# Kernel optimization log

Measured on AMD Instinct MI355X. Metric: run time of the kernel, lower is better.

Reference implementation:

```python
import jax, jax.numpy as jnp
import numpy as np

EPS = 1e-12

def lap_kernel(x, y, sigma):
    # x: [N,d], y: [M,d] -> exp(-||x-y|| / sigma), [N,M]
    D = jnp.sum((x[:, None, :] - y[None, :, :]) ** 2, axis=-1)
    return jnp.exp(-jnp.sqrt(jnp.maximum(D, EPS)) / sigma)

def setup_inputs() -> dict:
    key = jax.random.key(0)
    ks = jax.random.split(key, 8)
    N, L, NN, D, H = 20000, 7, 2048, 3, 16
    inp = {
        'x': jax.random.uniform(ks[0], (N, D), dtype=jnp.float32),
        'trial_points': jax.random.uniform(ks[1], (L, NN, D), dtype=jnp.float32),
        'W_emb': jax.random.normal(ks[2], (L, NN, H), dtype=jnp.float32),
        'alpha': 0.001 * jnp.ones((L,), dtype=jnp.float32),
        'sigma': 0.1 * jnp.ones((L,), dtype=jnp.float32),
    }
    dims = [L * H, 40, 40, 40, 40, 1]
    for i in range(5):
        fan_in = dims[i]
        kw = jax.random.fold_in(ks[3], i)
        inp[f'w{i+1}'] = (jax.random.normal(kw, (dims[i], dims[i+1]), dtype=jnp.float32)
                          / np.sqrt(fan_in).astype(np.float32))
        inp[f'b{i+1}'] = jnp.zeros((dims[i+1],), dtype=jnp.float32)
    return inp

def reference(x, trial_points, W_emb, alpha, sigma, w1, b1, w2, b2, w3, b3, w4, b4, w5, b5):
    n_lvls, n_nodes = trial_points.shape[0], trial_points.shape[1]
    I = jnp.eye(n_nodes, dtype=x.dtype)
    hs = []
    for l in range(n_lvls):  # fixed small loop over levels (7)
        xt = trial_points[l]                         # [NN, d]
        K_xx = lap_kernel(xt, xt, sigma[l])          # [NN, NN]
        a = jnp.linalg.solve(K_xx + alpha[l] * I, W_emb[l])  # ridge solve
        K_tx = lap_kernel(x, xt, sigma[l])           # [N, NN]
        hs.append(K_tx @ a)                          # [N, H]
    h = jnp.concatenate(hs, axis=-1)                 # [N, 7*H]
    z = jax.nn.relu(h @ w1 + b1)
    z = jax.nn.relu(z @ w2 + b2)
    z = jax.nn.relu(z @ w3 + b3)
    z = jax.nn.relu(z @ w4 + b4)
    return z @ w5 + b5
```

## Files before the change

kernel.cpp:

```cpp
#include <hip/hip_runtime.h>
#include <math.h>

#define NN   2048
#define NLVL 7
#define HD   16
#define HTOT 112
#define NB   64

__global__ __launch_bounds__(256) void build_K(
    const float* __restrict__ tp, const float* __restrict__ alpha,
    const float* __restrict__ sigma, float* __restrict__ K, int lvl0)
{
  int lz  = blockIdx.y;
  int lvl = lvl0 + lz;
  int idx = blockIdx.x * 256 + threadIdx.x;
  int i = idx >> 11, j = idx & (NN - 1);
  const float* xt = tp + (size_t)lvl * NN * 3;
  float xi0 = xt[i*3+0], xi1 = xt[i*3+1], xi2 = xt[i*3+2];
  float xj0 = xt[j*3+0], xj1 = xt[j*3+1], xj2 = xt[j*3+2];
  float d0 = xi0-xj0, d1 = xi1-xj1, d2 = xi2-xj2;
  float dd = d0*d0 + d1*d1 + d2*d2;
  float v = __expf(-sqrtf(fmaxf(dd, 1e-12f)) / sigma[lvl]);
  if (i == j) v += alpha[lvl];
  K[(size_t)lz*NN*NN + idx] = v;
}

__global__ __launch_bounds__(64) void chol_diag(float* __restrict__ K, int k)
{
  int lz = blockIdx.x;
  float* A = K + (size_t)lz * NN * NN;
  __shared__ float s[64][65];
  int tid = threadIdx.x;
  #pragma unroll 4
  for (int r = 0; r < 64; ++r)
    s[r][tid] = A[(size_t)(k + r) * NN + k + tid];
  __syncthreads();
  for (int j = 0; j < 64; ++j) {
    float djj = s[j][j];
    float inv = 1.0f / sqrtf(djj);
    if (tid > j) s[tid][j] *= inv;
    __syncthreads();
    if (tid > j) {
      float fr = s[tid][j];
      for (int p = j + 1; p <= tid; ++p)
        s[tid][p] -= fr * s[p][j];
    }
    __syncthreads();
  }
  s[tid][tid] = sqrtf(s[tid][tid]);
  __syncthreads();
  #pragma unroll 4
  for (int r = 0; r < 64; ++r)
    A[(size_t)(k + r) * NN + k + tid] = s[r][tid];
}

__global__ __launch_bounds__(128) void panel_trsm(float* __restrict__ K, int k)
{
  int lz = blockIdx.y;
  float* A = K + (size_t)lz * NN * NN;
  __shared__ float Ld[64][65];
  __shared__ float invd[64];
  __shared__ float P[128][65];
  int tid = threadIdx.x;
  for (int t = tid; t < 4096; t += 128)
    Ld[t >> 6][t & 63] = A[(size_t)(k + (t >> 6)) * NN + k + (t & 63)];
  int rbase = k + NB + blockIdx.x * 128;
  for (int t = tid; t < 128 * 64; t += 128) {
    int r = t >> 6, c = t & 63;
    if (rbase + r < NN) P[r][c] = A[(size_t)(rbase + r) * NN + k + c];
  }
  __syncthreads();
  if (tid < 64) invd[tid] = 1.0f / Ld[tid][tid];
  __syncthreads();
  int r = tid;
  if (rbase + r < NN) {
    for (int j = 0; j < 64; ++j) {
      float acc = P[r][j];
      for (int p = 0; p < j; ++p) acc -= Ld[j][p] * P[r][p];
      P[r][j] = acc * invd[j];
    }
  }
  __syncthreads();
  for (int t = tid; t < 128 * 64; t += 128) {
    int rr = t >> 6, c = t & 63;
    if (rbase + rr < NN) A[(size_t)(rbase + rr) * NN + k + c] = P[rr][c];
  }
}

__global__ __launch_bounds__(256) void syrk_update(float* __restrict__ K, int k)
{
  if (blockIdx.y > blockIdx.x) return;
  int lz = blockIdx.z;
  float* A = K + (size_t)lz * NN * NN;
  int i0 = k + NB + blockIdx.x * 64;
  int j0 = k + NB + blockIdx.y * 64;
  __shared__ __align__(16) float Asub[64][68];
  __shared__ __align__(16) float Bsub[64][68];
  int tid = threadIdx.x;
  for (int t = tid; t < 4096; t += 256) {
    int r = t >> 6, c = t & 63;
    Asub[r][c] = A[(size_t)(i0 + r) * NN + k + c];
    Bsub[r][c] = A[(size_t)(j0 + r) * NN + k + c];
  }
  __syncthreads();
  int tx = tid & 15, ty = tid >> 4;
  float acc[4][4] = {{0.f}};
  #pragma unroll
  for (int p4 = 0; p4 < 16; ++p4) {
    float4 av[4], bv[4];
    #pragma unroll
    for (int ii = 0; ii < 4; ++ii) av[ii] = *(const float4*)&Asub[ty*4+ii][p4*4];
    #pragma unroll
    for (int jj = 0; jj < 4; ++jj) bv[jj] = *(const float4*)&Bsub[tx*4+jj][p4*4];
    #pragma unroll
    for (int ii = 0; ii < 4; ++ii)
      #pragma unroll
      for (int jj = 0; jj < 4; ++jj)
        acc[ii][jj] += av[ii].x*bv[jj].x + av[ii].y*bv[jj].y
                     + av[ii].z*bv[jj].z + av[ii].w*bv[jj].w;
  }
  #pragma unroll
  for (int ii = 0; ii < 4; ++ii) {
    int row = i0 + ty*4 + ii;
    float4* cp = (float4*)&A[(size_t)row * NN + j0 + tx*4];
    float4 cv = *cp;
    cv.x -= acc[ii][0]; cv.y -= acc[ii][1]; cv.z -= acc[ii][2]; cv.w -= acc[ii][3];
    *cp = cv;
  }
}

__global__ __launch_bounds__(512) void trsm_diag_fwd(
    const float* __restrict__ K, float* __restrict__ Y, int kb)
{
  int lz = blockIdx.x;
  const float* L = K + (size_t)lz * NN * NN;
  float* y = Y + (size_t)lz * NN * HD;
  __shared__ float Ld1[64][65];
  __shared__ float L21[64][65];
  __shared__ float Ld2[64][65];
  __shared__ float yb[128][HD];
  int tid = threadIdx.x;
  for (int t = tid; t < 4096; t += 512) {
    int r = t >> 6, c = t & 63;
    Ld1[r][c] = L[(size_t)(kb + r) * NN + kb + c];
    L21[r][c] = L[(size_t)(kb + 64 + r) * NN + kb + c];
    Ld2[r][c] = L[(size_t)(kb + 64 + r) * NN + kb + 64 + c];
  }
  for (int t = tid; t < 128 * HD; t += 512)
    yb[t >> 4][t & 15] = y[(size_t)kb * HD + t];
  __syncthreads();
  if (tid < HD) {
    int c = tid;
    for (int j = 0; j < 64; ++j) {
      float acc = yb[j][c];
      for (int p = 0; p < j; ++p) acc -= Ld1[j][p] * yb[p][c];
      yb[j][c] = acc / Ld1[j][j];
    }
  }
  __syncthreads();
  {
    int o = tid;
    #pragma unroll
    for (int q = 0; q < 2; ++q, o += 512) {
      int r = o >> 4, c = o & 15;
      float acc = 0.f;
      #pragma unroll 16
      for (int p = 0; p < 64; ++p) acc += L21[r][p] * yb[p][c];
      yb[64 + r][c] -= acc;
    }
  }
  __syncthreads();
  if (tid < HD) {
    int c = tid;
    for (int j = 0; j < 64; ++j) {
      float acc = yb[64 + j][c];
      for (int p = 0; p < j; ++p) acc -= Ld2[j][p] * yb[64 + p][c];
      yb[64 + j][c] = acc / Ld2[j][j];
    }
  }
  __syncthreads();
  for (int t = tid; t < 128 * HD; t += 512)
    y[(size_t)kb * HD + t] = yb[t >> 4][t & 15];
}

__global__ __launch_bounds__(256) void trsm_upd_fwd(
    const float* __restrict__ K, float* __restrict__ Y, int kb)
{
  int lz = blockIdx.y;
  const float* L = K + (size_t)lz * NN * NN;
  float* y = Y + (size_t)lz * NN * HD;
  int i0 = kb + 128 + blockIdx.x * 64;
  __shared__ float Lt[64][129];
  __shared__ __align__(16) float yk[128][HD];
  int tid = threadIdx.x;
  for (int e = tid; e < 64 * 128; e += 256) {
    int r = e >> 7, p = e & 127;
    Lt[r][p] = L[(size_t)(i0 + r) * NN + kb + p];
  }
  for (int e = tid; e < 128 * HD; e += 256)
    yk[e >> 4][e & 15] = y[(size_t)kb * HD + e];
  __syncthreads();
  int row = tid & 63, cg = tid >> 6;
  float4 acc = make_float4(0.f, 0.f, 0.f, 0.f);
  #pragma unroll 8
  for (int p = 0; p < 128; ++p) {
    float l = Lt[row][p];
    float4 yv = *(const float4*)&yk[p][cg * 4];
    acc.x += l * yv.x; acc.y += l * yv.y; acc.z += l * yv.z; acc.w += l * yv.w;
  }
  float4* yp = (float4*)&y[(size_t)(i0 + row) * HD + cg * 4];
  float4 cv = *yp;
  cv.x -= acc.x; cv.y -= acc.y; cv.z -= acc.z; cv.w -= acc.w;
  *yp = cv;
}

__global__ __launch_bounds__(512) void trsm_diag_bwd(
    const float* __restrict__ K, float* __restrict__ Y, int kb)
{
  int lz = blockIdx.x;
  const float* L = K + (size_t)lz * NN * NN;
  float* y = Y + (size_t)lz * NN * HD;
  __shared__ float Ld1[64][65];
  __shared__ float L21[64][65];
  __shared__ float Ld2[64][65];
  __shared__ float yb[128][HD];
  int tid = threadIdx.x;
  for (int t = tid; t < 4096; t += 512) {
    int r = t >> 6, c = t & 63;
    Ld1[r][c] = L[(size_t)(kb + r) * NN + kb + c];
    L21[r][c] = L[(size_t)(kb + 64 + r) * NN + kb + c];
    Ld2[r][c] = L[(size_t)(kb + 64 + r) * NN + kb + 64 + c];
  }
  for (int t = tid; t < 128 * HD; t += 512)
    yb[t >> 4][t & 15] = y[(size_t)kb * HD + t];
  __syncthreads();
  if (tid < HD) {
    int c = tid;
    for (int j = 63; j >= 0; --j) {
      float acc = yb[64 + j][c];
      for (int p = j + 1; p < 64; ++p) acc -= Ld2[p][j] * yb[64 + p][c];
      yb[64 + j][c] = acc / Ld2[j][j];
    }
  }
  __syncthreads();
  {
    int o = tid;
    #pragma unroll
    for (int q = 0; q < 2; ++q, o += 512) {
      int r = o >> 4, c = o & 15;
      float acc = 0.f;
      #pragma unroll 16
      for (int p = 0; p < 64; ++p) acc += L21[p][r] * yb[64 + p][c];
      yb[r][c] -= acc;
    }
  }
  __syncthreads();
  if (tid < HD) {
    int c = tid;
    for (int j = 63; j >= 0; --j) {
      float acc = yb[j][c];
      for (int p = j + 1; p < 64; ++p) acc -= Ld1[p][j] * yb[p][c];
      yb[j][c] = acc / Ld1[j][j];
    }
  }
  __syncthreads();
  for (int t = tid; t < 128 * HD; t += 512)
    y[(size_t)kb * HD + t] = yb[t >> 4][t & 15];
}

__global__ __launch_bounds__(256) void trsm_upd_bwd(
    const float* __restrict__ K, float* __restrict__ Y, int kb)
{
  int lz = blockIdx.y;
  const float* L = K + (size_t)lz * NN * NN;
  float* y = Y + (size_t)lz * NN * HD;
  int i0 = blockIdx.x * 64;
  __shared__ float Lt[64][129];
  __shared__ __align__(16) float yk[128][HD];
  int tid = threadIdx.x;
  for (int e = tid; e < 64 * 128; e += 256) {
    int p = e >> 6, r = e & 63;
    Lt[r][p] = L[(size_t)(kb + p) * NN + i0 + r];
  }
  for (int e = tid; e < 128 * HD; e += 256)
    yk[e >> 4][e & 15] = y[(size_t)kb * HD + e];
  __syncthreads();
  int row = tid & 63, cg = tid >> 6;
  float4 acc = make_float4(0.f, 0.f, 0.f, 0.f);
  #pragma unroll 8
  for (int p = 0; p < 128; ++p) {
    float l = Lt[row][p];
    float4 yv = *(const float4*)&yk[p][cg * 4];
    acc.x += l * yv.x; acc.y += l * yv.y; acc.z += l * yv.z; acc.w += l * yv.w;
  }
  float4* yp = (float4*)&y[(size_t)(i0 + row) * HD + cg * 4];
  float4 cv = *yp;
  cv.x -= acc.x; cv.y -= acc.y; cv.z -= acc.z; cv.w -= acc.w;
  *yp = cv;
}

__global__ __launch_bounds__(256) void compute_h(
    const float* __restrict__ x, const float* __restrict__ tp,
    const float* __restrict__ A, const float* __restrict__ sigma,
    float* __restrict__ Ht, int N)
{
  int l = blockIdx.y;
  const float* xt = tp + (size_t)l * NN * 3;
  const float* al = A + (size_t)l * NN * HD;
  float inv_sigma = 1.0f / sigma[l];
  int tid = threadIdx.x;
  int r0 = blockIdx.x * 512 + tid;
  int r1 = r0 + 256;
  float x00=0.f,x01=0.f,x02=0.f, x10=0.f,x11=0.f,x12=0.f;
  if (r0 < N) { x00 = x[r0*3]; x01 = x[r0*3+1]; x02 = x[r0*3+2]; }
  if (r1 < N) { x10 = x[r1*3]; x11 = x[r1*3+1]; x12 = x[r1*3+2]; }
  __shared__ float sxt[128*3];
  __shared__ __align__(16) float sa[128*16];
  float acc0[16] = {0.f}; float acc1[16] = {0.f};
  for (int jc = 0; jc < NN; jc += 128) {
    __syncthreads();
    for (int t = tid; t < 384; t += 256)  sxt[t] = xt[jc*3 + t];
    for (int t = tid; t < 2048; t += 256) sa[t]  = al[jc*16 + t];
    __syncthreads();
    for (int jl = 0; jl < 128; ++jl) {
      float t0 = sxt[jl*3+0], t1 = sxt[jl*3+1], t2 = sxt[jl*3+2];
      float da = x00 - t0, db = x01 - t1, dc = x02 - t2;
      float d20 = da*da + db*db + dc*dc;
      da = x10 - t0; db = x11 - t1; dc = x12 - t2;
      float d21 = da*da + db*db + dc*dc;
      float k0 = __expf(-sqrtf(fmaxf(d20, 1e-12f)) * inv_sigma);
      float k1 = __expf(-sqrtf(fmaxf(d21, 1e-12f)) * inv_sigma);
      const float4* a4 = (const float4*)&sa[jl*16];
      #pragma unroll
      for (int q = 0; q < 4; ++q) {
        float4 av = a4[q];
        acc0[q*4+0] += k0*av.x; acc0[q*4+1] += k0*av.y;
        acc0[q*4+2] += k0*av.z; acc0[q*4+3] += k0*av.w;
        acc1[q*4+0] += k1*av.x; acc1[q*4+1] += k1*av.y;
        acc1[q*4+2] += k1*av.z; acc1[q*4+3] += k1*av.w;
      }
    }
  }
  if (r0 < N) {
    #pragma unroll
    for (int hh = 0; hh < 16; ++hh) Ht[(size_t)(l*HD + hh) * N + r0] = acc0[hh];
  }
  if (r1 < N) {
    #pragma unroll
    for (int hh = 0; hh < 16; ++hh) Ht[(size_t)(l*HD + hh) * N + r1] = acc1[hh];
  }
}

__global__ __launch_bounds__(256) void mlp_kernel(
    const float* __restrict__ Ht,
    const float* __restrict__ w1, const float* __restrict__ b1,
    const float* __restrict__ w2, const float* __restrict__ b2,
    const float* __restrict__ w3, const float* __restrict__ b3,
    const float* __restrict__ w4, const float* __restrict__ b4,
    const float* __restrict__ w5, const float* __restrict__ b5,
    float* __restrict__ out, int N)
{
  __shared__ __align__(16) float W1[HTOT*40];
  __shared__ __align__(16) float W2[1600];
  __shared__ __align__(16) float W3[1600];
  __shared__ __align__(16) float W4[1600];
  __shared__ float W5[40], B1[40], B2[40], B3[40], B4[40];
  __shared__ float B5s;
  int tid = threadIdx.x;
  for (int t = tid; t < HTOT*40; t += 256) W1[t] = w1[t];
  for (int t = tid; t < 1600; t += 256) { W2[t] = w2[t]; W3[t] = w3[t]; W4[t] = w4[t]; }
  if (tid < 40) { B1[tid]=b1[tid]; B2[tid]=b2[tid]; B3[tid]=b3[tid]; B4[tid]=b4[tid]; W5[tid]=w5[tid]; }
  if (tid == 0) B5s = b5[0];
  __syncthreads();
  int r = blockIdx.x * 256 + tid;
  if (r >= N) return;

  float za[40], zb[40];
  #pragma unroll
  for (int o = 0; o < 40; ++o) za[o] = B1[o];
  for (int i = 0; i < HTOT; ++i) {
    float hv = Ht[(size_t)i * N + r];
    const float4* wp = (const float4*)&W1[i*40];
    #pragma unroll
    for (int q = 0; q < 10; ++q) {
      float4 wv = wp[q];
      za[q*4+0] += hv*wv.x; za[q*4+1] += hv*wv.y; za[q*4+2] += hv*wv.z; za[q*4+3] += hv*wv.w;
    }
  }
  #pragma unroll
  for (int o = 0; o < 40; ++o) { za[o] = fmaxf(za[o], 0.f); zb[o] = B2[o]; }
  for (int i = 0; i < 40; ++i) {
    float hv = za[i];
    const float4* wp = (const float4*)&W2[i*40];
    #pragma unroll
    for (int q = 0; q < 10; ++q) {
      float4 wv = wp[q];
      zb[q*4+0] += hv*wv.x; zb[q*4+1] += hv*wv.y; zb[q*4+2] += hv*wv.z; zb[q*4+3] += hv*wv.w;
    }
  }
  #pragma unroll
  for (int o = 0; o < 40; ++o) { zb[o] = fmaxf(zb[o], 0.f); za[o] = B3[o]; }
  for (int i = 0; i < 40; ++i) {
    float hv = zb[i];
    const float4* wp = (const float4*)&W3[i*40];
    #pragma unroll
    for (int q = 0; q < 10; ++q) {
      float4 wv = wp[q];
      za[q*4+0] += hv*wv.x; za[q*4+1] += hv*wv.y; za[q*4+2] += hv*wv.z; za[q*4+3] += hv*wv.w;
    }
  }
  #pragma unroll
  for (int o = 0; o < 40; ++o) { za[o] = fmaxf(za[o], 0.f); zb[o] = B4[o]; }
  for (int i = 0; i < 40; ++i) {
    float hv = za[i];
    const float4* wp = (const float4*)&W4[i*40];
    #pragma unroll
    for (int q = 0; q < 10; ++q) {
      float4 wv = wp[q];
      zb[q*4+0] += hv*wv.x; zb[q*4+1] += hv*wv.y; zb[q*4+2] += hv*wv.z; zb[q*4+3] += hv*wv.w;
    }
  }
  float ov = B5s;
  #pragma unroll
  for (int o = 0; o < 40; ++o) ov += fmaxf(zb[o], 0.f) * W5[o];
  out[r] = ov;
}

static void run_chol_steps(float* K, int nl, hipStream_t stream)
{
  for (int k = 0; k < NN; k += NB) {
    chol_diag<<<nl, 64, 0, stream>>>(K, k);
    int m = NN - k - NB;
    if (m > 0) {
      panel_trsm<<<dim3((m + 127) / 128, nl), 128, 0, stream>>>(K, k);
      int t = m / 64;
      syrk_update<<<dim3(t, t, nl), 256, 0, stream>>>(K, k);
    }
  }
}

static void run_trsm_steps(const float* K, float* Y, int nl, hipStream_t stream)
{
  for (int kb = 0; kb < NN; kb += 128) {
    trsm_diag_fwd<<<nl, 512, 0, stream>>>(K, Y, kb);
    int m = NN - kb - 128;
    if (m > 0)
      trsm_upd_fwd<<<dim3(m / 64, nl), 256, 0, stream>>>(K, Y, kb);
  }
  for (int kb = NN - 128; kb >= 0; kb -= 128) {
    trsm_diag_bwd<<<nl, 512, 0, stream>>>(K, Y, kb);
    if (kb > 0)
      trsm_upd_bwd<<<dim3(kb / 64, nl), 256, 0, stream>>>(K, Y, kb);
  }
}

extern "C" void kernel_launch(void* const* d_in, const int* in_sizes, int n_in,
                              void* d_out, int out_size, void* d_ws, size_t ws_size,
                              hipStream_t stream)
{
  (void)n_in; (void)out_size;
  const float* x     = (const float*)d_in[0];
  const float* tp    = (const float*)d_in[1];
  const float* W     = (const float*)d_in[2];
  const float* alpha = (const float*)d_in[3];
  const float* sigma = (const float*)d_in[4];
  const float* w1 = (const float*)d_in[5];  const float* b1 = (const float*)d_in[6];
  const float* w2 = (const float*)d_in[7];  const float* b2 = (const float*)d_in[8];
  const float* w3 = (const float*)d_in[9];  const float* b3 = (const float*)d_in[10];
  const float* w4 = (const float*)d_in[11]; const float* b4 = (const float*)d_in[12];
  const float* w5 = (const float*)d_in[13]; const float* b5 = (const float*)d_in[14];
  float* out = (float*)d_out;
  int N = in_sizes[0] / 3;

  size_t kElems1 = (size_t)NN * NN;
  size_t aElems  = (size_t)NLVL * NN * HD;
  size_t hElems  = (size_t)N * HTOT;
  size_t need7   = (7 * kElems1 + aElems + hElems) * sizeof(float);
  bool batched = ws_size >= need7;
  int nlK = batched ? NLVL : 1;

  float* K = (float*)d_ws;
  float* A = K + (size_t)nlK * kElems1;
  float* H = A + aElems;

  hipMemcpyAsync(A, W, aElems * sizeof(float), hipMemcpyDeviceToDevice, stream);

  if (batched) {
    build_K<<<dim3((unsigned)(kElems1 / 256), NLVL), 256, 0, stream>>>(tp, alpha, sigma, K, 0);
    run_chol_steps(K, NLVL, stream);
    run_trsm_steps(K, A, NLVL, stream);
  } else {
    for (int l = 0; l < NLVL; ++l) {
      build_K<<<dim3((unsigned)(kElems1 / 256), 1), 256, 0, stream>>>(tp, alpha, sigma, K, l);
      run_chol_steps(K, 1, stream);
      run_trsm_steps(K, A + (size_t)l * NN * HD, 1, stream);
    }
  }

  compute_h<<<dim3((N + 511) / 512, NLVL), 256, 0, stream>>>(x, tp, A, sigma, H, N);
  mlp_kernel<<<(N + 255) / 256, 256, 0, stream>>>(H, w1, b1, w2, b2, w3, b3, w4, b4, w5, b5, out, N);
}
```

Baseline: 9.309 ms.

## Fuse kernel build, Cholesky and triangular solves into one cooperative persistent kernel

Replaces the many per-step launches for building the kernel matrices, the blocked Cholesky factorisation and the forward/backward triangular solves with a single cooperative grid kernel that uses grid-wide syncs between phases. Diagonal factorisation is fused into the trailing SYRK step, and diagonal solves are fused with their updates on dedicated blocks per level. This targets launch overhead and idle gaps on the long serial dependency chain, at the cost of grid-sync latency and limited occupancy. It also changes compute_h to one row per thread with more blocks, and falls back to the old path if the cooperative launch fails.

```diff
diff --git a/kernel.cpp b/kernel.cpp
--- a/kernel.cpp
+++ b/kernel.cpp
@@ -1,11 +1,429 @@
 #include <hip/hip_runtime.h>
+#include <hip/hip_cooperative_groups.h>
 #include <math.h>
 
-#define NN   2048
-#define NLVL 7
-#define HD   16
-#define HTOT 112
-#define NB   64
+namespace cg = cooperative_groups;
+
+#define NN     2048
+#define NLVL   7
+#define HD     16
+#define HTOT   112
+#define NB     64
+
+#define LDS_FLOATS 10368
+
+__device__ void chol64_lds(float* s, int tid)
+{
+  for (int j = 0; j < 64; ++j) {
+    float pj = s[j*68+j];
+    __syncthreads();
+    float inv = 1.0f / sqrtf(pj);
+    if (tid == j) s[j*68+j] = sqrtf(pj);
+    else if (tid > j && tid < 64) s[tid*68+j] *= inv;
+    __syncthreads();
+    int rr = j + 1 + (tid >> 2);
+    if (rr < 64) {
+      float lr = s[rr*68+j];
+      for (int c = j + 1 + (tid & 3); c <= rr; c += 4)
+        s[rr*68+c] -= lr * s[c*68+j];
+    }
+    __syncthreads();
+  }
+}
+
+__device__ void panel_tile(float* __restrict__ A, int k, int r0, float* lds, int tid)
+{
+  float* Ld = lds; float* P = lds + 4160; float* invd = lds + 8320;
+  for (int t = tid; t < 4096; t += 256) {
+    int r = t >> 6, c = t & 63;
+    Ld[r*65+c] = A[(size_t)(k + r) * NN + k + c];
+    P [r*65+c] = A[(size_t)(r0 + r) * NN + k + c];
+  }
+  __syncthreads();
+  if (tid < 64) invd[tid] = 1.0f / Ld[tid*65+tid];
+  __syncthreads();
+  if (tid < 64) {
+    int r = tid;
+    for (int j = 0; j < 64; ++j) {
+      float acc = P[r*65+j];
+      for (int p = 0; p < j; ++p) acc -= Ld[j*65+p] * P[r*65+p];
+      P[r*65+j] = acc * invd[j];
+    }
+  }
+  __syncthreads();
+  for (int t = tid; t < 4096; t += 256) {
+    int r = t >> 6, c = t & 63;
+    A[(size_t)(r0 + r) * NN + k + c] = P[r*65+c];
+  }
+  __syncthreads();
+}
+
+__device__ void syrk_tile(float* __restrict__ A, int k, int i0, int j0,
+                          float* lds, int tid, bool fuse)
+{
+  float* As = lds; float* Bs = lds + 4352;
+  for (int t = tid; t < 4096; t += 256) {
+    int r = t >> 6, c = t & 63;
+    As[r*68+c] = A[(size_t)(i0 + r) * NN + k + c];
+    Bs[r*68+c] = A[(size_t)(j0 + r) * NN + k + c];
+  }
+  __syncthreads();
+  int tx = tid & 15, ty = tid >> 4;
+  float acc[4][4] = {{0.f}};
+  #pragma unroll
+  for (int p4 = 0; p4 < 16; ++p4) {
+    float4 av[4], bv[4];
+    #pragma unroll
+    for (int ii = 0; ii < 4; ++ii) av[ii] = *(const float4*)&As[(ty*4+ii)*68 + p4*4];
+    #pragma unroll
+    for (int jj = 0; jj < 4; ++jj) bv[jj] = *(const float4*)&Bs[(tx*4+jj)*68 + p4*4];
+    #pragma unroll
+    for (int ii = 0; ii < 4; ++ii)
+      #pragma unroll
+      for (int jj = 0; jj < 4; ++jj)
+        acc[ii][jj] += av[ii].x*bv[jj].x + av[ii].y*bv[jj].y
+                     + av[ii].z*bv[jj].z + av[ii].w*bv[jj].w;
+  }
+  if (!fuse) {
+    #pragma unroll
+    for (int ii = 0; ii < 4; ++ii) {
+      float4* cp = (float4*)&A[(size_t)(i0 + ty*4 + ii) * NN + j0 + tx*4];
+      float4 cv = *cp;
+      cv.x -= acc[ii][0]; cv.y -= acc[ii][1]; cv.z -= acc[ii][2]; cv.w -= acc[ii][3];
+      *cp = cv;
+    }
+    __syncthreads();
+  } else {
+    float4 cv[4];
+    #pragma unroll
+    for (int ii = 0; ii < 4; ++ii) {
+      cv[ii] = *(const float4*)&A[(size_t)(i0 + ty*4 + ii) * NN + j0 + tx*4];
+      cv[ii].x -= acc[ii][0]; cv[ii].y -= acc[ii][1];
+      cv[ii].z -= acc[ii][2]; cv[ii].w -= acc[ii][3];
+    }
+    __syncthreads();
+    #pragma unroll
+    for (int ii = 0; ii < 4; ++ii)
+      *(float4*)&As[(ty*4+ii)*68 + tx*4] = cv[ii];
+    __syncthreads();
+    chol64_lds(As, tid);
+    for (int t = tid; t < 4096; t += 256) {
+      int r = t >> 6, c = t & 63;
+      A[(size_t)(i0 + r) * NN + i0 + c] = As[r*68+c];
+    }
+    __syncthreads();
+  }
+}
+
+__device__ void solve128_fwd(const float* __restrict__ L, int kb, float* lds, int tid)
+{
+  float* LA = lds; float* LB = lds + 4160; float* yb = lds + 8320;
+  for (int t = tid; t < 4096; t += 256) {
+    int r = t >> 6, c = t & 63;
+    LA[r*65+c] = L[(size_t)(kb + r) * NN + kb + c];
+    LB[r*65+c] = L[(size_t)(kb + 64 + r) * NN + kb + c];
+  }
+  __syncthreads();
+  if (tid < HD) {
+    int c = tid;
+    for (int j = 0; j < 64; ++j) {
+      float acc = yb[j*HD + c];
+      for (int p = 0; p < j; ++p) acc -= LA[j*65+p] * yb[p*HD + c];
+      yb[j*HD + c] = acc / LA[j*65+j];
+    }
+  }
+  __syncthreads();
+  for (int o = tid; o < 1024; o += 256) {
+    int r = o >> 4, c = o & 15;
+    float acc = 0.f;
+    #pragma unroll 8
+    for (int p = 0; p < 64; ++p) acc += LB[r*65+p] * yb[p*HD + c];
+    yb[(64+r)*HD + c] -= acc;
+  }
+  for (int t = tid; t < 4096; t += 256) {
+    int r = t >> 6, c = t & 63;
+    LA[r*65+c] = L[(size_t)(kb + 64 + r) * NN + (kb + 64) + c];
+  }
+  __syncthreads();
+  if (tid < HD) {
+    int c = tid;
+    for (int j = 0; j < 64; ++j) {
+      float acc = yb[(64+j)*HD + c];
+      for (int p = 0; p < j; ++p) acc -= LA[j*65+p] * yb[(64+p)*HD + c];
+      yb[(64+j)*HD + c] = acc / LA[j*65+j];
+    }
+  }
+  __syncthreads();
+}
+
+__device__ void solve128_bwd(const float* __restrict__ L, int kb, float* lds, int tid)
+{
+  float* LA = lds; float* LB = lds + 4160; float* yb = lds + 8320;
+  for (int t = tid; t < 4096; t += 256) {
+    int r = t >> 6, c = t & 63;
+    LA[r*65+c] = L[(size_t)(kb + 64 + r) * NN + (kb + 64) + c];
+    LB[r*65+c] = L[(size_t)(kb + 64 + r) * NN + kb + c];
+  }
+  __syncthreads();
+  if (tid < HD) {
+    int c = tid;
+    for (int j = 63; j >= 0; --j) {
+      float acc = yb[(64+j)*HD + c];
+      for (int p = j + 1; p < 64; ++p) acc -= LA[p*65+j] * yb[(64+p)*HD + c];
+      yb[(64+j)*HD + c] = acc / LA[j*65+j];
+    }
+  }
+  __syncthreads();
+  for (int o = tid; o < 1024; o += 256) {
+    int r = o >> 4, c = o & 15;
+    float acc = 0.f;
+    #pragma unroll 8
+    for (int p = 0; p < 64; ++p) acc += LB[p*65+r] * yb[(64+p)*HD + c];
+    yb[r*HD + c] -= acc;
+  }
+  for (int t = tid; t < 4096; t += 256) {
+    int r = t >> 6, c = t & 63;
+    LA[r*65+c] = L[(size_t)(kb + r) * NN + kb + c];
+  }
+  __syncthreads();
+  if (tid < HD) {
+    int c = tid;
+    for (int j = 63; j >= 0; --j) {
+      float acc = yb[j*HD + c];
+      for (int p = j + 1; p < 64; ++p) acc -= LA[p*65+j] * yb[p*HD + c];
+      yb[j*HD + c] = acc / LA[j*65+j];
+    }
+  }
+  __syncthreads();
+}
+
+__device__ void upd_tile_fwd_c(const float* __restrict__ L, float* __restrict__ yl,
+                               int kb, int r0, float* lds, int tid)
+{
+  float* Lt = lds; float* yk = lds + 8320;
+  for (int e = tid; e < 8192; e += 256) {
+    int r = e >> 7, p = e & 127;
+    Lt[r*129+p] = L[(size_t)(r0 + r) * NN + kb + p];
+  }
+  for (int e = tid; e < 2048; e += 256) yk[e] = yl[(size_t)kb * HD + e];
+  __syncthreads();
+  int row = tid & 63, cgp = tid >> 6;
+  float4 acc = make_float4(0.f,0.f,0.f,0.f);
+  #pragma unroll 8
+  for (int p = 0; p < 128; ++p) {
+    float l = Lt[row*129+p];
+    float4 yv = *(const float4*)&yk[p*HD + cgp*4];
+    acc.x += l*yv.x; acc.y += l*yv.y; acc.z += l*yv.z; acc.w += l*yv.w;
+  }
+  float4* yp = (float4*)&yl[(size_t)(r0 + row) * HD + cgp*4];
+  float4 cv = *yp;
+  cv.x -= acc.x; cv.y -= acc.y; cv.z -= acc.z; cv.w -= acc.w;
+  *yp = cv;
+  __syncthreads();
+}
+
+__device__ void upd_tile_bwd_c(const float* __restrict__ L, float* __restrict__ yl,
+                               int kb, int r0, float* lds, int tid)
+{
+  float* Lt = lds; float* yk = lds + 8320;
+  for (int e = tid; e < 8192; e += 256) {
+    int p = e >> 6, r = e & 63;
+    Lt[r*129+p] = L[(size_t)(kb + p) * NN + r0 + r];
+  }
+  for (int e = tid; e < 2048; e += 256) yk[e] = yl[(size_t)kb * HD + e];
+  __syncthreads();
+  int row = tid & 63, cgp = tid >> 6;
+  float4 acc = make_float4(0.f,0.f,0.f,0.f);
+  #pragma unroll 8
+  for (int p = 0; p < 128; ++p) {
+    float l = Lt[row*129+p];
+    float4 yv = *(const float4*)&yk[p*HD + cgp*4];
+    acc.x += l*yv.x; acc.y += l*yv.y; acc.z += l*yv.z; acc.w += l*yv.w;
+  }
+  float4* yp = (float4*)&yl[(size_t)(r0 + row) * HD + cgp*4];
+  float4 cv = *yp;
+  cv.x -= acc.x; cv.y -= acc.y; cv.z -= acc.z; cv.w -= acc.w;
+  *yp = cv;
+  __syncthreads();
+}
+
+__device__ void fwd_step_diag(const float* __restrict__ L, float* __restrict__ yl,
+                              int kb, float* lds, int tid)
+{
+  float* Lt = lds; float* yb = lds + 8320;
+  int row = tid & 63, cgp = tid >> 6;
+  float4 ynew[2];
+  #pragma unroll
+  for (int h = 0; h < 2; ++h) {
+    int r0 = kb + 128 + h*64;
+    for (int e = tid; e < 8192; e += 256) {
+      int r = e >> 7, p = e & 127;
+      Lt[r*129+p] = L[(size_t)(r0 + r) * NN + kb + p];
+    }
+    __syncthreads();
+    float4 acc = make_float4(0.f,0.f,0.f,0.f);
+    #pragma unroll 8
+    for (int p = 0; p < 128; ++p) {
+      float l = Lt[row*129+p];
+      float4 yv = *(const float4*)&yb[p*HD + cgp*4];
+      acc.x += l*yv.x; acc.y += l*yv.y; acc.z += l*yv.z; acc.w += l*yv.w;
+    }
+    float4 cv = *(const float4*)&yl[(size_t)(r0 + row) * HD + cgp*4];
+    ynew[h] = make_float4(cv.x-acc.x, cv.y-acc.y, cv.z-acc.z, cv.w-acc.w);
+    __syncthreads();
+  }
+  *(float4*)&yb[row*HD + cgp*4]      = ynew[0];
+  *(float4*)&yb[(64+row)*HD + cgp*4] = ynew[1];
+  __syncthreads();
+  solve128_fwd(L, kb + 128, lds, tid);
+  for (int t = tid; t < 2048; t += 256)
+    yl[(size_t)(kb + 128) * HD + t] = yb[t];
+}
+
+__device__ void bwd_step_diag(const float* __restrict__ L, float* __restrict__ yl,
+                              int kb, float* lds, int tid)
+{
+  float* Lt = lds; float* yb = lds + 8320;
+  int row = tid & 63, cgp = tid >> 6;
+  float4 ynew[2];
+  #pragma unroll
+  for (int h = 0; h < 2; ++h) {
+    int r0 = kb - 128 + h*64;
+    for (int e = tid; e < 8192; e += 256) {
+      int p = e >> 6, r = e & 63;
+      Lt[r*129+p] = L[(size_t)(kb + p) * NN + r0 + r];
+    }
+    __syncthreads();
+    float4 acc = make_float4(0.f,0.f,0.f,0.f);
+    #pragma unroll 8
+    for (int p = 0; p < 128; ++p) {
+      float l = Lt[row*129+p];
+      float4 yv = *(const float4*)&yb[p*HD + cgp*4];
+      acc.x += l*yv.x; acc.y += l*yv.y; acc.z += l*yv.z; acc.w += l*yv.w;
+    }
+    float4 cv = *(const float4*)&yl[(size_t)(r0 + row) * HD + cgp*4];
+    ynew[h] = make_float4(cv.x-acc.x, cv.y-acc.y, cv.z-acc.z, cv.w-acc.w);
+    __syncthreads();
+  }
+  *(float4*)&yb[row*HD + cgp*4]      = ynew[0];
+  *(float4*)&yb[(64+row)*HD + cgp*4] = ynew[1];
+  __syncthreads();
+  solve128_bwd(L, kb - 128, lds, tid);
+  for (int t = tid; t < 2048; t += 256)
+    yl[(size_t)(kb - 128) * HD + t] = yb[t];
+}
+
+__global__ __launch_bounds__(256, 2) void solve_all(
+    float* __restrict__ K, float* __restrict__ Y,
+    const float* __restrict__ tp, const float* __restrict__ alpha,
+    const float* __restrict__ sigma, const float* __restrict__ W, int nl)
+{
+  cg::grid_group gg = cg::this_grid();
+  __shared__ __align__(16) float lds[LDS_FLOATS];
+  const int w = blockIdx.x, G = gridDim.x, tid = threadIdx.x;
+
+  for (int lz = 0; lz < nl; ++lz) {
+    const float* xt = tp + (size_t)lz * NN * 3;
+    const float a_ = alpha[lz];
+    const float is_ = 1.0f / sigma[lz];
+    float* Kl = K + (size_t)lz * NN * NN;
+    for (int idx = w * 256 + tid; idx < NN*NN; idx += G * 256) {
+      int i = idx >> 11, j = idx & (NN - 1);
+      float d0 = xt[i*3]-xt[j*3], d1 = xt[i*3+1]-xt[j*3+1], d2 = xt[i*3+2]-xt[j*3+2];
+      float dd = d0*d0 + d1*d1 + d2*d2;
+      float v = __expf(-sqrtf(fmaxf(dd, 1e-12f)) * is_);
+      if (i == j) v += a_;
+      Kl[idx] = v;
+    }
+  }
+  for (int t = w * 256 + tid; t < nl * NN * HD; t += G * 256) Y[t] = W[t];
+  gg.sync();
+
+  if (w < nl) {
+    float* A = K + (size_t)w * NN * NN;
+    for (int t = tid; t < 4096; t += 256)
+      lds[(t >> 6)*68 + (t & 63)] = A[(size_t)(t >> 6) * NN + (t & 63)];
+    __syncthreads();
+    chol64_lds(lds, tid);
+    for (int t = tid; t < 4096; t += 256)
+      A[(size_t)(t >> 6) * NN + (t & 63)] = lds[(t >> 6)*68 + (t & 63)];
+  }
+  gg.sync();
+
+  for (int k = 0; k + 64 < NN; k += 64) {
+    int t64 = (NN - k - 64) >> 6;
+    for (int g = w; g < nl * t64; g += G) {
+      int lz = g / t64, rt = g - lz * t64;
+      panel_tile(K + (size_t)lz * NN * NN, k, k + 64 + rt * 64, lds, tid);
+    }
+    gg.sync();
+    int T = t64 * (t64 + 1) / 2;
+    if (w < nl) {
+      syrk_tile(K + (size_t)w * NN * NN, k, k + 64, k + 64, lds, tid, true);
+    } else if (T > 1) {
+      int nd = nl * (T - 1);
+      for (int g = w - nl; g < nd; g += G - nl) {
+        int lz = g / (T - 1);
+        int idx = 1 + g - lz * (T - 1);
+        int i = (int)((sqrtf(8.0f * idx + 1.0f) - 1.0f) * 0.5f);
+        while ((i + 1) * (i + 2) / 2 <= idx) ++i;
+        while (i * (i + 1) / 2 > idx) --i;
+        int j = idx - i * (i + 1) / 2;
+        syrk_tile(K + (size_t)lz * NN * NN, k, k + 64 + i * 64, k + 64 + j * 64,
+                  lds, tid, false);
+      }
+    }
+    gg.sync();
+  }
+
+  if (w < nl) {
+    float* yb = lds + 8320;
+    float* yl = Y + (size_t)w * NN * HD;
+    for (int t = tid; t < 2048; t += 256) yb[t] = yl[t];
+    solve128_fwd(K + (size_t)w * NN * NN, 0, lds, tid);
+    for (int t = tid; t < 2048; t += 256) yl[t] = yb[t];
+  }
+  gg.sync();
+  for (int kb = 0; kb + 128 < NN; kb += 128) {
+    if (w < nl) {
+      fwd_step_diag(K + (size_t)w * NN * NN, Y + (size_t)w * NN * HD, kb, lds, tid);
+    } else {
+      int ntot = (NN - kb - 256) >> 6;
+      if (ntot > 0) {
+        for (int g = w - nl; g < nl * ntot; g += G - nl) {
+          int lz = g / ntot, rt = g - lz * ntot;
+          upd_tile_fwd_c(K + (size_t)lz * NN * NN, Y + (size_t)lz * NN * HD,
+                         kb, kb + 256 + rt * 64, lds, tid);
+        }
+      }
+    }
+    gg.sync();
+  }
+
+  if (w < nl) {
+    float* yb = lds + 8320;
+    float* yl = Y + (size_t)w * NN * HD;
+    solve128_bwd(K + (size_t)w * NN * NN, NN - 128, lds, tid);
+    for (int t = tid; t < 2048; t += 256)
+      yl[(size_t)(NN - 128) * HD + t] = yb[t];
+  }
+  gg.sync();
+  for (int kb = NN - 128; kb >= 128; kb -= 128) {
+    if (w < nl) {
+      bwd_step_diag(K + (size_t)w * NN * NN, Y + (size_t)w * NN * HD, kb, lds, tid);
+    } else {
+      int ntot = (kb - 128) >> 6;
+      if (ntot > 0) {
+        for (int g = w - nl; g < nl * ntot; g += G - nl) {
+          int lz = g / ntot, rt = g - lz * ntot;
+          upd_tile_bwd_c(K + (size_t)lz * NN * NN, Y + (size_t)lz * NN * HD,
+                         kb, rt * 64, lds, tid);
+        }
+      }
+    }
+    gg.sync();
+  }
+}
 
 __global__ __launch_bounds__(256) void build_K(
     const float* __restrict__ tp, const float* __restrict__ alpha,
@@ -16,9 +434,7 @@
   int idx = blockIdx.x * 256 + threadIdx.x;
   int i = idx >> 11, j = idx & (NN - 1);
   const float* xt = tp + (size_t)lvl * NN * 3;
-  float xi0 = xt[i*3+0], xi1 = xt[i*3+1], xi2 = xt[i*3+2];
-  float xj0 = xt[j*3+0], xj1 = xt[j*3+1], xj2 = xt[j*3+2];
-  float d0 = xi0-xj0, d1 = xi1-xj1, d2 = xi2-xj2;
+  float d0 = xt[i*3]-xt[j*3], d1 = xt[i*3+1]-xt[j*3+1], d2 = xt[i*3+2]-xt[j*3+2];
   float dd = d0*d0 + d1*d1 + d2*d2;
   float v = __expf(-sqrtf(fmaxf(dd, 1e-12f)) / sigma[lvl]);
   if (i == j) v += alpha[lvl];
@@ -200,15 +616,15 @@
   for (int e = tid; e < 128 * HD; e += 256)
     yk[e >> 4][e & 15] = y[(size_t)kb * HD + e];
   __syncthreads();
-  int row = tid & 63, cg = tid >> 6;
+  int row = tid & 63, cg2 = tid >> 6;
   float4 acc = make_float4(0.f, 0.f, 0.f, 0.f);
   #pragma unroll 8
   for (int p = 0; p < 128; ++p) {
     float l = Lt[row][p];
-    float4 yv = *(const float4*)&yk[p][cg * 4];
+    float4 yv = *(const float4*)&yk[p][cg2 * 4];
     acc.x += l * yv.x; acc.y += l * yv.y; acc.z += l * yv.z; acc.w += l * yv.w;
   }
-  float4* yp = (float4*)&y[(size_t)(i0 + row) * HD + cg * 4];
+  float4* yp = (float4*)&y[(size_t)(i0 + row) * HD + cg2 * 4];
   float4 cv = *yp;
   cv.x -= acc.x; cv.y -= acc.y; cv.z -= acc.z; cv.w -= acc.w;
   *yp = cv;
@@ -285,15 +701,15 @@
   for (int e = tid; e < 128 * HD; e += 256)
     yk[e >> 4][e & 15] = y[(size_t)kb * HD + e];
   __syncthreads();
-  int row = tid & 63, cg = tid >> 6;
+  int row = tid & 63, cg2 = tid >> 6;
   float4 acc = make_float4(0.f, 0.f, 0.f, 0.f);
   #pragma unroll 8
   for (int p = 0; p < 128; ++p) {
     float l = Lt[row][p];
-    float4 yv = *(const float4*)&yk[p][cg * 4];
+    float4 yv = *(const float4*)&yk[p][cg2 * 4];
     acc.x += l * yv.x; acc.y += l * yv.y; acc.z += l * yv.z; acc.w += l * yv.w;
   }
-  float4* yp = (float4*)&y[(size_t)(i0 + row) * HD + cg * 4];
+  float4* yp = (float4*)&y[(size_t)(i0 + row) * HD + cg2 * 4];
   float4 cv = *yp;
   cv.x -= acc.x; cv.y -= acc.y; cv.z -= acc.z; cv.w -= acc.w;
   *yp = cv;
@@ -309,45 +725,35 @@
   const float* al = A + (size_t)l * NN * HD;
   float inv_sigma = 1.0f / sigma[l];
   int tid = threadIdx.x;
-  int r0 = blockIdx.x * 512 + tid;
-  int r1 = r0 + 256;
-  float x00=0.f,x01=0.f,x02=0.f, x10=0.f,x11=0.f,x12=0.f;
-  if (r0 < N) { x00 = x[r0*3]; x01 = x[r0*3+1]; x02 = x[r0*3+2]; }
-  if (r1 < N) { x10 = x[r1*3]; x11 = x[r1*3+1]; x12 = x[r1*3+2]; }
+  int r = blockIdx.x * 256 + tid;
+  float x0 = 0.f, x1 = 0.f, x2 = 0.f;
+  if (r < N) { x0 = x[r*3]; x1 = x[r*3+1]; x2 = x[r*3+2]; }
   __shared__ float sxt[128*3];
   __shared__ __align__(16) float sa[128*16];
-  float acc0[16] = {0.f}; float acc1[16] = {0.f};
+  float acc[16] = {0.f};
   for (int jc = 0; jc < NN; jc += 128) {
     __syncthreads();
     for (int t = tid; t < 384; t += 256)  sxt[t] = xt[jc*3 + t];
     for (int t = tid; t < 2048; t += 256) sa[t]  = al[jc*16 + t];
     __syncthreads();
+    #pragma unroll 2
     for (int jl = 0; jl < 128; ++jl) {
       float t0 = sxt[jl*3+0], t1 = sxt[jl*3+1], t2 = sxt[jl*3+2];
-      float da = x00 - t0, db = x01 - t1, dc = x02 - t2;
-      float d20 = da*da + db*db + dc*dc;
-      da = x10 - t0; db = x11 - t1; dc = x12 - t2;
-      float d21 = da*da + db*db + dc*dc;
-      float k0 = __expf(-sqrtf(fmaxf(d20, 1e-12f)) * inv_sigma);
-      float k1 = __expf(-sqrtf(fmaxf(d21, 1e-12f)) * inv_sigma);
+      float da = x0 - t0, db = x1 - t1, dc = x2 - t2;
+      float d2 = da*da + db*db + dc*dc;
+      float kv = __expf(-sqrtf(fmaxf(d2, 1e-12f)) * inv_sigma);
       const float4* a4 = (const float4*)&sa[jl*16];
       #pragma unroll
       for (int q = 0; q < 4; ++q) {
         float4 av = a4[q];
-        acc0[q*4+0] += k0*av.x; acc0[q*4+1] += k0*av.y;
-        acc0[q*4+2] += k0*av.z; acc0[q*4+3] += k0*av.w;
-        acc1[q*4+0] += k1*av.x; acc1[q*4+1] += k1*av.y;
-        acc1[q*4+2] += k1*av.z; acc1[q*4+3] += k1*av.w;
+        acc[q*4+0] += kv*av.x; acc[q*4+1] += kv*av.y;
+        acc[q*4+2] += kv*av.z; acc[q*4+3] += kv*av.w;
       }
     }
   }
-  if (r0 < N) {
-    #pragma unroll
-    for (int hh = 0; hh < 16; ++hh) Ht[(size_t)(l*HD + hh) * N + r0] = acc0[hh];
-  }
-  if (r1 < N) {
-    #pragma unroll
-    for (int hh = 0; hh < 16; ++hh) Ht[(size_t)(l*HD + hh) * N + r1] = acc1[hh];
+  if (r < N) {
+    #pragma unroll
+    for (int hh = 0; hh < 16; ++hh) Ht[(size_t)(l*HD + hh) * N + r] = acc[hh];
   }
 }
 
@@ -475,28 +881,54 @@
   size_t kElems1 = (size_t)NN * NN;
   size_t aElems  = (size_t)NLVL * NN * HD;
   size_t hElems  = (size_t)N * HTOT;
-  size_t need7   = (7 * kElems1 + aElems + hElems) * sizeof(float);
+  size_t need7   = (NLVL * kElems1 + aElems + hElems) * sizeof(float);
   bool batched = ws_size >= need7;
-  int nlK = batched ? NLVL : 1;
-
-  float* K = (float*)d_ws;
-  float* A = K + (size_t)nlK * kElems1;
-  float* H = A + aElems;
-
-  hipMemcpyAsync(A, W, aElems * sizeof(float), hipMemcpyDeviceToDevice, stream);
-
+
+  float* K; float* Y; float* H;
   if (batched) {
-    build_K<<<dim3((unsigned)(kElems1 / 256), NLVL), 256, 0, stream>>>(tp, alpha, sigma, K, 0);
-    run_chol_steps(K, NLVL, stream);
-    run_trsm_steps(K, A, NLVL, stream);
+    K = (float*)d_ws; Y = K + NLVL * kElems1; H = Y + aElems;
   } else {
-    for (int l = 0; l < NLVL; ++l) {
-      build_K<<<dim3((unsigned)(kElems1 / 256), 1), 256, 0, stream>>>(tp, alpha, sigma, K, l);
-      run_chol_steps(K, 1, stream);
-      run_trsm_steps(K, A + (size_t)l * NN * HD, 1, stream);
-    }
-  }
-
-  compute_h<<<dim3((N + 511) / 512, NLVL), 256, 0, stream>>>(x, tp, A, sigma, H, N);
-  mlp_kernel<<<(N + 255) / 256, 256, 0, stream>>>(H, w1, b1, w2, b2, w3, b3, w4, b4, w5, b5, out, N);
-}
+    K = (float*)d_ws; Y = K + kElems1;        H = Y + aElems;
+  }
+
+  bool coop_done = false;
+  if (batched) {
+    int dev = 0;
+    (void)hipGetDevice(&dev);
+    hipDeviceProp_t prop;
+    hipError_t pe = hipGetDeviceProperties(&prop, dev);
+    int maxB = 0;
+    hipError_t oe = hipOccupancyMaxActiveBlocksPerMultiprocessor(&maxB, solve_all, 256, 0);
+    if (pe == hipSuccess && oe == hipSuccess) {
+      long coopMax = (long)maxB * (long)prop.multiProcessorCount;
+      int G = (int)(coopMax < 512 ? coopMax : 512);
+      if (G >= 16) {
+        int nlv = NLVL;
+        void* args[] = { (void*)&K, (void*)&Y, (void*)&tp, (void*)&alpha,
+                         (void*)&sigma, (void*)&W, (void*)&nlv };
+        hipError_t le = hipLaunchCooperativeKernel((void*)solve_all, dim3(G),
+                                                   dim3(256), args, 0, stream);
+        if (le == hipSuccess) coop_done = true;
+      }
+    }
+  }
+
+  if (!coop_done) {
+    hipMemcpyAsync(Y, W, aElems * sizeof(float), hipMemcpyDeviceToDevice, stream);
+    if (batched) {
+      build_K<<<dim3((unsigned)(kElems1 / 256), NLVL), 256, 0, stream>>>(tp, alpha, sigma, K, 0);
+      run_chol_steps(K, NLVL, stream);
+      run_trsm_steps(K, Y, NLVL, stream);
+    } else {
+      for (int l = 0; l < NLVL; ++l) {
+        build_K<<<dim3((unsigned)(kElems1 / 256), 1), 256, 0, stream>>>(tp, alpha, sigma, K, l);
+        run_chol_steps(K, 1, stream);
+        run_trsm_steps(K, Y + (size_t)l * NN * HD, 1, stream);
+      }
+    }
+  }
+
+  compute_h<<<dim3((N + 255) / 256, NLVL), 256, 0, stream>>>(x, tp, Y, sigma, H, N);
+  mlp_kernel<<<(N + 255) / 256, 256, 0, stream>>>(H, w1, b1, w2, b2, w3, b3,
+                                                  w4, b4, w5, b5, out, N);
+}
```

Result: slower. 14.04 ms (+50.8%).
